# Optimization experiments

Hardware: AMD Instinct MI355X
Metric: run time of the kernel (lower is better)

## Reference

```python
import jax, jax.numpy as jnp
from jax import lax
import numpy as np

W_SSIM = 0.5
W_SMOOTH = 0.1
W_LR = 1.0
C1 = 0.01 ** 2
C2 = 0.03 ** 2


def avg3(x):
    # 3x3 stride-1 VALID average pool (matches F.avg_pool2d(x, 3, 1))
    return lax.reduce_window(x, 0.0, lax.add, (1, 1, 3, 3), (1, 1, 1, 1), 'VALID') / 9.0


def resize_ac(img, oh, ow):
    # bilinear resize with align_corners=True, separable gathers
    B, C, H, W = img.shape
    ys = jnp.linspace(0.0, H - 1.0, oh)
    xs = jnp.linspace(0.0, W - 1.0, ow)
    y0 = jnp.floor(ys).astype(jnp.int32); y1 = jnp.minimum(y0 + 1, H - 1); wy = ys - y0
    x0 = jnp.floor(xs).astype(jnp.int32); x1 = jnp.minimum(x0 + 1, W - 1); wx = xs - x0
    r = img[:, :, y0, :] * (1.0 - wy)[None, None, :, None] + img[:, :, y1, :] * wy[None, None, :, None]
    return r[:, :, :, x0] * (1.0 - wx) + r[:, :, :, x1] * wx


def warp_h(img, disp, sign):
    # horizontal bilinear warp: sample img at x + sign*disp (disp in units of image width),
    # align_corners=True pixel mapping, zeros padding outside the image.
    B, C, H, W = img.shape
    xb = jnp.linspace(0.0, 1.0, W)
    px = (xb[None, None, :] + sign * disp[:, 0, :, :]) * (W - 1)  # [B,H,W] pixel coords
    x0 = jnp.floor(px); f = px - x0
    x0i = x0.astype(jnp.int32); x1i = x0i + 1
    v0 = ((x0i >= 0) & (x0i < W)).astype(img.dtype)
    v1 = ((x1i >= 0) & (x1i < W)).astype(img.dtype)
    i0 = jnp.broadcast_to(jnp.clip(x0i, 0, W - 1)[:, None], (B, C, H, W))
    i1 = jnp.broadcast_to(jnp.clip(x1i, 0, W - 1)[:, None], (B, C, H, W))
    g0 = jnp.take_along_axis(img, i0, axis=3)
    g1 = jnp.take_along_axis(img, i1, axis=3)
    return g0 * (v0 * (1.0 - f))[:, None] + g1 * (v1 * f)[:, None]


def ssim(x, y):
    mu_x = avg3(x); mu_y = avg3(y)
    sig_x = avg3(x * x) - mu_x ** 2
    sig_y = avg3(y * y) - mu_y ** 2
    sig_xy = avg3(x * y) - mu_x * mu_y
    s = ((2 * mu_x * mu_y + C1) * (2 * sig_xy + C2)) / ((mu_x ** 2 + mu_y ** 2 + C1) * (sig_x + sig_y + C2))
    return jnp.clip((1.0 - s) / 2.0, 0.0, 1.0)


def smoothness(disp, img):
    dgx = disp[:, :, :, :-1] - disp[:, :, :, 1:]
    dgy = disp[:, :, :-1, :] - disp[:, :, 1:, :]
    igx = img[:, :, :, :-1] - img[:, :, :, 1:]
    igy = img[:, :, :-1, :] - img[:, :, 1:, :]
    wx = jnp.exp(-jnp.mean(jnp.abs(igx), axis=1, keepdims=True))
    wy = jnp.exp(-jnp.mean(jnp.abs(igy), axis=1, keepdims=True))
    return jnp.mean(jnp.abs(dgx * wx)) + jnp.mean(jnp.abs(dgy * wy))


def compute_loss(disps, left, right):
    B, _, H, W = left.shape
    img_loss = 0.0
    lr_loss = 0.0
    sm_loss = 0.0
    for i, d in enumerate(disps):
        r = 2 ** i
        h, w = H // r, W // r
        lpy = left if i == 0 else resize_ac(left, h, w)
        rpy = right if i == 0 else resize_ac(right, h, w)
        dl = d[:, 0:1]; dr = d[:, 1:2]
        left_est = warp_h(rpy, dl, -1.0)
        right_est = warp_h(lpy, dr, 1.0)
        rl_disp = warp_h(dr, dl, -1.0)
        lr_disp = warp_h(dl, dr, 1.0)
        l1_l = jnp.mean(jnp.abs(left_est - lpy))
        l1_r = jnp.mean(jnp.abs(right_est - rpy))
        ss_l = jnp.mean(ssim(left_est, lpy))
        ss_r = jnp.mean(ssim(right_est, rpy))
        img_loss = img_loss + W_SSIM * ss_l + (1 - W_SSIM) * l1_l + W_SSIM * ss_r + (1 - W_SSIM) * l1_r
        lr_loss = lr_loss + jnp.mean(jnp.abs(rl_disp - dl)) + jnp.mean(jnp.abs(lr_disp - dr))
        sm_loss = sm_loss + (smoothness(dl, lpy) + smoothness(dr, rpy)) / r
    return img_loss + W_SMOOTH * sm_loss + W_LR * lr_loss


def setup_inputs() -> dict:
    key = jax.random.key(0)
    ks = jax.random.split(key, 6)
    B, H, W = 16, 384, 768
    inp = {}
    for i in range(4):
        r = 2 ** i
        # disparities in units of image width; scaled to realistic ~[0, 0.1]
        inp[f'disp{i}'] = jax.random.uniform(ks[i], (B, 2, H // r, W // r), dtype=jnp.float32) * 0.1
    inp['left_image'] = jax.random.uniform(ks[4], (B, 3, H, W), dtype=jnp.float32)
    inp['right_image'] = jax.random.uniform(ks[5], (B, 3, H, W), dtype=jnp.float32)
    return inp


def reference(disp0, disp1, disp2, disp3, left_image, right_image):
    return compute_loss([disp0, disp1, disp2, disp3], left_image, right_image)
```

## Files before the change

kernel.cpp:

```cpp
#include <hip/hip_runtime.h>
#include <math.h>

#define C1F 1.0e-4f
#define C2F 9.0e-4f
#define TX 32
#define TY 8


struct ScaleArgs {
    const float* disp;
    const float* lp;
    const float* rp;
    int h, w, nx, ny, blk0;
};

__device__ __forceinline__ float2 f2(float v) { return make_float2(v, v); }
__device__ __forceinline__ float2 f2abs(float2 a) {
    return make_float2(fabsf(a.x), fabsf(a.y));
}

__device__ __forceinline__ void warp_coeffs(float px, int W, int& i0, int& i1,
                                            float& w0, float& w1) {
    float x0f = floorf(px);
    float f = px - x0f;
    int x0i = (int)x0f;
    int x1i = x0i + 1;
    float v0 = (x0i >= 0 && x0i < W) ? 1.f : 0.f;
    float v1 = (x1i >= 0 && x1i < W) ? 1.f : 0.f;
    i0 = min(max(x0i, 0), W - 1);
    i1 = min(max(x1i, 0), W - 1);
    w0 = v0 * (1.f - f);
    w1 = v1 * f;
}

template<int N>
__device__ __forceinline__ void block_acc(const float* vals, float* gacc) {
    __shared__ float sacc[N];
    if (threadIdx.x < N) sacc[threadIdx.x] = 0.f;
    __syncthreads();
#pragma unroll
    for (int k = 0; k < N; ++k) {
        float v = vals[k];
#pragma unroll
        for (int off = 32; off > 0; off >>= 1) v += __shfl_down(v, off, 64);
        if ((threadIdx.x & 63) == 0) atomicAdd(&sacc[k], v);
    }
    __syncthreads();
    if (threadIdx.x < N) atomicAdd(&gacc[threadIdx.x], sacc[threadIdx.x]);
}

__global__ void __launch_bounds__(256, 4)
k_resize_all(const float* __restrict__ left, const float* __restrict__ right,
             float* __restrict__ lo1, float* __restrict__ ro1,
             float* __restrict__ lo2, float* __restrict__ ro2,
             float* __restrict__ lo3, float* __restrict__ ro3,
             float* __restrict__ acc,
             int B, int H, int W,
             long long n1, long long n2, long long n3) {
    if (blockIdx.x == gridDim.x - 1 && threadIdx.x < 64) acc[threadIdx.x] = 0.f;
    long long idx = (long long)blockIdx.x * blockDim.x + threadIdx.x;
    int oh, ow;
    float* lo;
    float* ro;
    if (idx < n1) {
        oh = H / 2; ow = W / 2; lo = lo1; ro = ro1;
    } else if (idx < n1 + n2) {
        idx -= n1; oh = H / 4; ow = W / 4; lo = lo2; ro = ro2;
    } else if (idx < n1 + n2 + n3) {
        idx -= n1 + n2; oh = H / 8; ow = W / 8; lo = lo3; ro = ro3;
    } else {
        return;
    }
    long long half = (long long)B * 3 * oh * ow;
    const float* src = left;
    float* dst = lo;
    if (idx >= half) { src = right; dst = ro; idx -= half; }
    int x = (int)(idx % ow);
    long long t = idx / ow;
    int y = (int)(t % oh);
    t /= oh;
    int c = (int)(t % 3);
    int b = (int)(t / 3);
    float sy = (float)(H - 1) / (float)(oh - 1);
    float sx = (float)(W - 1) / (float)(ow - 1);
    float fy = y * sy;
    float fx = x * sx;
    int y0 = (int)floorf(fy); float wy = fy - (float)y0;
    int x0 = (int)floorf(fx); float wx = fx - (float)x0;
    int y1 = min(y0 + 1, H - 1); y0 = min(y0, H - 1);
    int x1 = min(x0 + 1, W - 1); x0 = min(x0, W - 1);
    const float* p = src + (((long long)b * 3 + c) * H) * W;
    float a00 = p[(long long)y0 * W + x0];
    float a10 = p[(long long)y1 * W + x0];
    float a01 = p[(long long)y0 * W + x1];
    float a11 = p[(long long)y1 * W + x1];
    float r0 = a00 * (1.f - wy) + a10 * wy;
    float r1 = a01 * (1.f - wy) + a11 * wy;
    dst[(((long long)b * 3 + c) * oh + y) * ow + x] = r0 * (1.f - wx) + r1 * wx;
}

__global__ void __launch_bounds__(256, 4)
k_fused_all(ScaleArgs s0, ScaleArgs s1, ScaleArgs s2, ScaleArgs s3,
            float* __restrict__ accbase) {
    __shared__ float4 simg[3][(TY + 2) * (TX + 2)];
    __shared__ float2 sdisp[(TY + 2) * (TX + 2)];

    ScaleArgs sa;
    int scale;
    {
        int blk = blockIdx.x;
        if (blk >= s3.blk0)      { sa = s3; scale = 3; }
        else if (blk >= s2.blk0) { sa = s2; scale = 2; }
        else if (blk >= s1.blk0) { sa = s1; scale = 1; }
        else                     { sa = s0; scale = 0; }
    }
    const int h = sa.h, w = sa.w;
    const float* __restrict__ disp = sa.disp;
    const float* __restrict__ lpy = sa.lp;
    const float* __restrict__ rpy = sa.rp;
    float* acc = accbase + scale * 8;

    int t = blockIdx.x - sa.blk0;
    const int tileX = t % sa.nx;
    int t2 = t / sa.nx;
    const int tileY = t2 % sa.ny;
    const int b = t2 / sa.ny;

    const int xo0 = tileX * TX;
    const int yo0 = tileY * TY;
    const int tid = threadIdx.x;
    const float Wm1 = (float)(w - 1);
    const float invWm1 = 1.f / Wm1;

    const float* dl_base = disp + ((long long)b * 2 + 0) * h * w;
    const float* dr_base = disp + ((long long)b * 2 + 1) * h * w;

    for (int i = tid; i < (TY + 2) * (TX + 2); i += 256) {
        int sx = i % (TX + 2);
        int sy = i / (TX + 2);
        int x = min(max(xo0 - 1 + sx, 0), w - 1);
        int y = min(max(yo0 - 1 + sy, 0), h - 1);
        const float* dl_row = dl_base + (long long)y * w;
        const float* dr_row = dr_base + (long long)y * w;
        float dl = dl_row[x], dr = dr_row[x];
        sdisp[i] = make_float2(dl, dr);
        float xb = (float)x * invWm1;
        int i0L, i1L; float w0L, w1L;
        warp_coeffs((xb - dl) * Wm1, w, i0L, i1L, w0L, w1L);
        int i0R, i1R; float w0R, w1R;
        warp_coeffs((xb + dr) * Wm1, w, i0R, i1R, w0R, w1R);
#pragma unroll
        for (int c = 0; c < 3; ++c) {
            const float* lrow = lpy + (((long long)b * 3 + c) * h + y) * w;
            const float* rrow = rpy + (((long long)b * 3 + c) * h + y) * w;
            float lv = lrow[x], rv = rrow[x];
            float le = rrow[i0L] * w0L + rrow[i1L] * w1L;
            float re = lrow[i0R] * w0R + lrow[i1R] * w1R;
            simg[c][i] = make_float4(le, re, lv, rv);
        }
    }
    __syncthreads();

    float sums[8] = {0.f, 0.f, 0.f, 0.f, 0.f, 0.f, 0.f, 0.f};
    const int tx = tid % TX, ty = tid / TX;
    const int x = xo0 + tx, y = yo0 + ty;
    if (x < w && y < h) {
        const int s = (ty + 1) * (TX + 2) + (tx + 1);
        float2 dd = sdisp[s];
        float dl = dd.x, dr = dd.y;
#pragma unroll
        for (int c = 0; c < 3; ++c) {
            float4 v = simg[c][s];
            float2 a = make_float2(v.x, v.y);
            float2 bb = make_float2(v.z, v.w);
            float2 d = f2abs(a - bb);
            sums[0] += d.x;
            sums[1] += d.y;
        }
        {
            float xb = (float)x * invWm1;
            int i0, i1; float w0, w1;
            warp_coeffs((xb - dl) * Wm1, w, i0, i1, w0, w1);
            const float* dr_row = dr_base + (long long)y * w;
            float rl = dr_row[i0] * w0 + dr_row[i1] * w1;
            sums[2] += fabsf(rl - dl);
            warp_coeffs((xb + dr) * Wm1, w, i0, i1, w0, w1);
            const float* dl_row = dl_base + (long long)y * w;
            float lr = dl_row[i0] * w0 + dl_row[i1] * w1;
            sums[3] += fabsf(lr - dr);
        }
        const float third = 1.f / 3.f;
        if (x < w - 1) {
            float2 d1 = sdisp[s + 1];
            float2 alr = f2(0.f);
#pragma unroll
            for (int c = 0; c < 3; ++c) {
                float4 v = simg[c][s];
                float4 v1 = simg[c][s + 1];
                alr = alr + f2abs(make_float2(v.z, v.w) - make_float2(v1.z, v1.w));
            }
            sums[4] += fabsf((dl - d1.x) * expf(-alr.x * third)) +
                       fabsf((dr - d1.y) * expf(-alr.y * third));
        }
        if (y < h - 1) {
            float2 d1 = sdisp[s + (TX + 2)];
            float2 alr = f2(0.f);
#pragma unroll
            for (int c = 0; c < 3; ++c) {
                float4 v = simg[c][s];
                float4 v1 = simg[c][s + (TX + 2)];
                alr = alr + f2abs(make_float2(v.z, v.w) - make_float2(v1.z, v1.w));
            }
            sums[5] += fabsf((dl - d1.x) * expf(-alr.x * third)) +
                       fabsf((dr - d1.y) * expf(-alr.y * third));
        }
        if (x >= 1 && x <= w - 2 && y >= 1 && y <= h - 2) {
            const float2 inv9 = f2(1.f / 9.f);
            const float2 c1 = f2(C1F), c2 = f2(C2F);
            const float2 two = f2(2.f), one = f2(1.f), half_ = f2(0.5f);
#pragma unroll 1
            for (int c = 0; c < 3; ++c) {
                float2 sX = f2(0.f), sY = f2(0.f);
                float2 sXX = f2(0.f), sYY = f2(0.f), sXY = f2(0.f);
#pragma unroll
                for (int dy = 0; dy < 3; ++dy) {
#pragma unroll
                    for (int dx = 0; dx < 3; ++dx) {
                        float4 v = simg[c][(ty + dy) * (TX + 2) + (tx + dx)];
                        float2 a = make_float2(v.x, v.y);
                        float2 bb = make_float2(v.z, v.w);
                        sX = sX + a;
                        sY = sY + bb;
                        sXX = sXX + a * a;
                        sYY = sYY + bb * bb;
                        sXY = sXY + a * bb;
                    }
                }
                float2 mx = sX * inv9, my = sY * inv9;
                float2 vx = sXX * inv9 - mx * mx;
                float2 vy = sYY * inv9 - my * my;
                float2 vxy = sXY * inv9 - mx * my;
                float2 num = (two * mx * my + c1) * (two * vxy + c2);
                float2 den = (mx * mx + my * my + c1) * (vx + vy + c2);
                float2 ss = make_float2(num.x / den.x, num.y / den.y);
                float2 v = (one - ss) * half_;
                sums[6] += fminf(fmaxf(v.x, 0.f), 1.f);
                sums[7] += fminf(fmaxf(v.y, 0.f), 1.f);
            }
        }
    }
    block_acc<8>(sums, acc);
}

__global__ void k_final(const float* __restrict__ acc, float* __restrict__ out,
                        int B, int H, int W) {
    if (threadIdx.x != 0 || blockIdx.x != 0) return;
    float img = 0.f, lr = 0.f, sm = 0.f;
    for (int i = 0; i < 4; ++i) {
        int r = 1 << i;
        int h = H / r, w = W / r;
        const float* a = acc + i * 8;
        float Nl1 = (float)B * 3.f * (float)h * (float)w;
        float Nss = (float)B * 3.f * (float)(h - 2) * (float)(w - 2);
        float Nlr = (float)B * (float)h * (float)w;
        float Nsx = (float)B * (float)h * (float)(w - 1);
        float Nsy = (float)B * (float)(h - 1) * (float)w;
        img += 0.5f * (a[6] / Nss) + 0.5f * (a[0] / Nl1)
             + 0.5f * (a[7] / Nss) + 0.5f * (a[1] / Nl1);
        lr += a[2] / Nlr + a[3] / Nlr;
        sm += (a[4] / Nsx + a[5] / Nsy) / (float)r;
    }
    out[0] = img + 0.1f * sm + 1.0f * lr;
}

extern "C" void kernel_launch(void* const* d_in, const int* in_sizes, int n_in,
                              void* d_out, int out_size, void* d_ws, size_t ws_size,
                              hipStream_t stream) {
    const int B = 16, H = 384, W = 768;
    const float* disp[4] = {(const float*)d_in[0], (const float*)d_in[1],
                            (const float*)d_in[2], (const float*)d_in[3]};
    const float* left = (const float*)d_in[4];
    const float* right = (const float*)d_in[5];
    float* out = (float*)d_out;

    float* acc = (float*)d_ws;
    float* pyr = acc + 256;
    long long sz1 = (long long)B * 3 * (H / 2) * (W / 2);
    long long sz2 = (long long)B * 3 * (H / 4) * (W / 4);
    long long sz3 = (long long)B * 3 * (H / 8) * (W / 8);
    float* lp1 = pyr;
    float* rp1 = lp1 + sz1;
    float* lp2 = rp1 + sz1;
    float* rp2 = lp2 + sz2;
    float* lp3 = rp2 + sz2;
    float* rp3 = lp3 + sz3;

    const int TB = 256;

    {
        long long n1 = 2 * sz1, n2 = 2 * sz2, n3 = 2 * sz3;
        long long nt = n1 + n2 + n3;
        hipLaunchKernelGGL(k_resize_all, dim3((unsigned)((nt + TB - 1) / TB)), dim3(TB), 0, stream,
                           left, right, lp1, rp1, lp2, rp2, lp3, rp3, acc,
                           B, H, W, n1, n2, n3);
    }

    {
        const float* lp[4] = {left, lp1, lp2, lp3};
        const float* rp[4] = {right, rp1, rp2, rp3};
        ScaleArgs sa[4];
        int blk0 = 0;
        for (int i = 0; i < 4; ++i) {
            int r = 1 << i;
            int h = H / r, w = W / r;
            sa[i].disp = disp[i];
            sa[i].lp = lp[i];
            sa[i].rp = rp[i];
            sa[i].h = h;
            sa[i].w = w;
            sa[i].nx = w / TX;
            sa[i].ny = h / TY;
            sa[i].blk0 = blk0;
            blk0 += sa[i].nx * sa[i].ny * B;
        }
        hipLaunchKernelGGL(k_fused_all, dim3((unsigned)blk0), dim3(TB), 0, stream,
                           sa[0], sa[1], sa[2], sa[3], acc);
    }
    hipLaunchKernelGGL(k_final, dim3(1), dim3(64), 0, stream, acc, out, B, H, W);
}
```

Measured before the change: 506.0 us.

## Fuse pyramid resize into loss kernel, sampling full-res images on the fly

Result: slower. 542.3 us (+7.2%).

```diff
diff --git a/kernel.cpp b/kernel.cpp
--- a/kernel.cpp
+++ b/kernel.cpp
@@ -9,8 +9,6 @@
 
 struct ScaleArgs {
     const float* disp;
-    const float* lp;
-    const float* rp;
     int h, w, nx, ny, blk0;
 };
 
@@ -33,6 +31,41 @@
     w1 = v1 * f;
 }
 
+__device__ __forceinline__ float3 bil3(const float* __restrict__ img,
+                                       long long bOff, long long cStride,
+                                       int FW, int y0, int y1, float wy,
+                                       int xs, float sx) {
+    float fx = (float)xs * sx;
+    int x0 = (int)floorf(fx);
+    float wx = fx - (float)x0;
+    int x1 = min(x0 + 1, FW - 1);
+    x0 = min(x0, FW - 1);
+    const float* p0 = img + bOff + (long long)y0 * FW;
+    const float* p1 = img + bOff + (long long)y1 * FW;
+    float3 r;
+    {
+        float a00 = p0[x0], a10 = p1[x0], a01 = p0[x1], a11 = p1[x1];
+        float r0 = a00 * (1.f - wy) + a10 * wy;
+        float r1 = a01 * (1.f - wy) + a11 * wy;
+        r.x = r0 * (1.f - wx) + r1 * wx;
+    }
+    p0 += cStride; p1 += cStride;
+    {
+        float a00 = p0[x0], a10 = p1[x0], a01 = p0[x1], a11 = p1[x1];
+        float r0 = a00 * (1.f - wy) + a10 * wy;
+        float r1 = a01 * (1.f - wy) + a11 * wy;
+        r.y = r0 * (1.f - wx) + r1 * wx;
+    }
+    p0 += cStride; p1 += cStride;
+    {
+        float a00 = p0[x0], a10 = p1[x0], a01 = p0[x1], a11 = p1[x1];
+        float r0 = a00 * (1.f - wy) + a10 * wy;
+        float r1 = a01 * (1.f - wy) + a11 * wy;
+        r.z = r0 * (1.f - wx) + r1 * wx;
+    }
+    return r;
+}
+
 template<int N>
 __device__ __forceinline__ void block_acc(const float* vals, float* gacc) {
     __shared__ float sacc[N];
@@ -49,59 +82,14 @@
     if (threadIdx.x < N) atomicAdd(&gacc[threadIdx.x], sacc[threadIdx.x]);
 }
 
-__global__ void __launch_bounds__(256, 4)
-k_resize_all(const float* __restrict__ left, const float* __restrict__ right,
-             float* __restrict__ lo1, float* __restrict__ ro1,
-             float* __restrict__ lo2, float* __restrict__ ro2,
-             float* __restrict__ lo3, float* __restrict__ ro3,
-             float* __restrict__ acc,
-             int B, int H, int W,
-             long long n1, long long n2, long long n3) {
-    if (blockIdx.x == gridDim.x - 1 && threadIdx.x < 64) acc[threadIdx.x] = 0.f;
-    long long idx = (long long)blockIdx.x * blockDim.x + threadIdx.x;
-    int oh, ow;
-    float* lo;
-    float* ro;
-    if (idx < n1) {
-        oh = H / 2; ow = W / 2; lo = lo1; ro = ro1;
-    } else if (idx < n1 + n2) {
-        idx -= n1; oh = H / 4; ow = W / 4; lo = lo2; ro = ro2;
-    } else if (idx < n1 + n2 + n3) {
-        idx -= n1 + n2; oh = H / 8; ow = W / 8; lo = lo3; ro = ro3;
-    } else {
-        return;
-    }
-    long long half = (long long)B * 3 * oh * ow;
-    const float* src = left;
-    float* dst = lo;
-    if (idx >= half) { src = right; dst = ro; idx -= half; }
-    int x = (int)(idx % ow);
-    long long t = idx / ow;
-    int y = (int)(t % oh);
-    t /= oh;
-    int c = (int)(t % 3);
-    int b = (int)(t / 3);
-    float sy = (float)(H - 1) / (float)(oh - 1);
-    float sx = (float)(W - 1) / (float)(ow - 1);
-    float fy = y * sy;
-    float fx = x * sx;
-    int y0 = (int)floorf(fy); float wy = fy - (float)y0;
-    int x0 = (int)floorf(fx); float wx = fx - (float)x0;
-    int y1 = min(y0 + 1, H - 1); y0 = min(y0, H - 1);
-    int x1 = min(x0 + 1, W - 1); x0 = min(x0, W - 1);
-    const float* p = src + (((long long)b * 3 + c) * H) * W;
-    float a00 = p[(long long)y0 * W + x0];
-    float a10 = p[(long long)y1 * W + x0];
-    float a01 = p[(long long)y0 * W + x1];
-    float a11 = p[(long long)y1 * W + x1];
-    float r0 = a00 * (1.f - wy) + a10 * wy;
-    float r1 = a01 * (1.f - wy) + a11 * wy;
-    dst[(((long long)b * 3 + c) * oh + y) * ow + x] = r0 * (1.f - wx) + r1 * wx;
+__global__ void k_zero(float* acc) {
+    if (threadIdx.x < 64) acc[threadIdx.x] = 0.f;
 }
 
 __global__ void __launch_bounds__(256, 4)
 k_fused_all(ScaleArgs s0, ScaleArgs s1, ScaleArgs s2, ScaleArgs s3,
-            float* __restrict__ accbase) {
+            const float* __restrict__ fleft, const float* __restrict__ fright,
+            int FH, int FW, float* __restrict__ accbase) {
     __shared__ float4 simg[3][(TY + 2) * (TX + 2)];
     __shared__ float2 sdisp[(TY + 2) * (TX + 2)];
 
@@ -116,8 +104,6 @@
     }
     const int h = sa.h, w = sa.w;
     const float* __restrict__ disp = sa.disp;
-    const float* __restrict__ lpy = sa.lp;
-    const float* __restrict__ rpy = sa.rp;
     float* acc = accbase + scale * 8;
 
     int t = blockIdx.x - sa.blk0;
@@ -134,12 +120,14 @@
 
     const float* dl_base = disp + ((long long)b * 2 + 0) * h * w;
     const float* dr_base = disp + ((long long)b * 2 + 1) * h * w;
+    const long long cStride = (long long)FH * FW;
+    const long long bOff = (long long)b * 3 * cStride;
 
     for (int i = tid; i < (TY + 2) * (TX + 2); i += 256) {
-        int sx = i % (TX + 2);
-        int sy = i / (TX + 2);
-        int x = min(max(xo0 - 1 + sx, 0), w - 1);
-        int y = min(max(yo0 - 1 + sy, 0), h - 1);
+        int sx_ = i % (TX + 2);
+        int sy_ = i / (TX + 2);
+        int x = min(max(xo0 - 1 + sx_, 0), w - 1);
+        int y = min(max(yo0 - 1 + sy_, 0), h - 1);
         const float* dl_row = dl_base + (long long)y * w;
         const float* dr_row = dr_base + (long long)y * w;
         float dl = dl_row[x], dr = dr_row[x];
@@ -149,14 +137,36 @@
         warp_coeffs((xb - dl) * Wm1, w, i0L, i1L, w0L, w1L);
         int i0R, i1R; float w0R, w1R;
         warp_coeffs((xb + dr) * Wm1, w, i0R, i1R, w0R, w1R);
-#pragma unroll
-        for (int c = 0; c < 3; ++c) {
-            const float* lrow = lpy + (((long long)b * 3 + c) * h + y) * w;
-            const float* rrow = rpy + (((long long)b * 3 + c) * h + y) * w;
-            float lv = lrow[x], rv = rrow[x];
-            float le = rrow[i0L] * w0L + rrow[i1L] * w1L;
-            float re = lrow[i0R] * w0R + lrow[i1R] * w1R;
-            simg[c][i] = make_float4(le, re, lv, rv);
+        if (scale == 0) {
+#pragma unroll
+            for (int c = 0; c < 3; ++c) {
+                const float* lrow = fleft + bOff + c * cStride + (long long)y * FW;
+                const float* rrow = fright + bOff + c * cStride + (long long)y * FW;
+                float lv = lrow[x], rv = rrow[x];
+                float le = rrow[i0L] * w0L + rrow[i1L] * w1L;
+                float re = lrow[i0R] * w0R + lrow[i1R] * w1R;
+                simg[c][i] = make_float4(le, re, lv, rv);
+            }
+        } else {
+            float syc = (float)(FH - 1) / (float)(h - 1);
+            float sxc = (float)(FW - 1) / (float)(w - 1);
+            float fy = (float)y * syc;
+            int y0 = (int)floorf(fy);
+            float wy = fy - (float)y0;
+            int y1 = min(y0 + 1, FH - 1);
+            y0 = min(y0, FH - 1);
+            float3 lv3 = bil3(fleft, bOff, cStride, FW, y0, y1, wy, x, sxc);
+            float3 rv3 = bil3(fright, bOff, cStride, FW, y0, y1, wy, x, sxc);
+            float3 rg0 = bil3(fright, bOff, cStride, FW, y0, y1, wy, i0L, sxc);
+            float3 rg1 = bil3(fright, bOff, cStride, FW, y0, y1, wy, i1L, sxc);
+            float3 lg0 = bil3(fleft, bOff, cStride, FW, y0, y1, wy, i0R, sxc);
+            float3 lg1 = bil3(fleft, bOff, cStride, FW, y0, y1, wy, i1R, sxc);
+            simg[0][i] = make_float4(rg0.x * w0L + rg1.x * w1L,
+                                     lg0.x * w0R + lg1.x * w1R, lv3.x, rv3.x);
+            simg[1][i] = make_float4(rg0.y * w0L + rg1.y * w1L,
+                                     lg0.y * w0R + lg1.y * w1R, lv3.y, rv3.y);
+            simg[2][i] = make_float4(rg0.z * w0L + rg1.z * w1L,
+                                     lg0.z * w0R + lg1.z * w1R, lv3.z, rv3.z);
         }
     }
     __syncthreads();
@@ -282,40 +292,18 @@
     const float* left = (const float*)d_in[4];
     const float* right = (const float*)d_in[5];
     float* out = (float*)d_out;
-
     float* acc = (float*)d_ws;
-    float* pyr = acc + 256;
-    long long sz1 = (long long)B * 3 * (H / 2) * (W / 2);
-    long long sz2 = (long long)B * 3 * (H / 4) * (W / 4);
-    long long sz3 = (long long)B * 3 * (H / 8) * (W / 8);
-    float* lp1 = pyr;
-    float* rp1 = lp1 + sz1;
-    float* lp2 = rp1 + sz1;
-    float* rp2 = lp2 + sz2;
-    float* lp3 = rp2 + sz2;
-    float* rp3 = lp3 + sz3;
 
     const int TB = 256;
-
-    {
-        long long n1 = 2 * sz1, n2 = 2 * sz2, n3 = 2 * sz3;
-        long long nt = n1 + n2 + n3;
-        hipLaunchKernelGGL(k_resize_all, dim3((unsigned)((nt + TB - 1) / TB)), dim3(TB), 0, stream,
-                           left, right, lp1, rp1, lp2, rp2, lp3, rp3, acc,
-                           B, H, W, n1, n2, n3);
-    }
-
-    {
-        const float* lp[4] = {left, lp1, lp2, lp3};
-        const float* rp[4] = {right, rp1, rp2, rp3};
+    hipLaunchKernelGGL(k_zero, dim3(1), dim3(64), 0, stream, acc);
+
+    {
         ScaleArgs sa[4];
         int blk0 = 0;
         for (int i = 0; i < 4; ++i) {
             int r = 1 << i;
             int h = H / r, w = W / r;
             sa[i].disp = disp[i];
-            sa[i].lp = lp[i];
-            sa[i].rp = rp[i];
             sa[i].h = h;
             sa[i].w = w;
             sa[i].nx = w / TX;
@@ -324,7 +312,7 @@
             blk0 += sa[i].nx * sa[i].ny * B;
         }
         hipLaunchKernelGGL(k_fused_all, dim3((unsigned)blk0), dim3(TB), 0, stream,
-                           sa[0], sa[1], sa[2], sa[3], acc);
+                           sa[0], sa[1], sa[2], sa[3], left, right, H, W, acc);
     }
     hipLaunchKernelGGL(k_final, dim3(1), dim3(64), 0, stream, acc, out, B, H, W);
 }
```

## Overlap full-resolution loss tiles with pyramid resize in one launch

Applied to the files above, without the earlier changes.

After: 514.0 us. No clear change (+1.6%).

```diff
diff --git a/kernel.cpp b/kernel.cpp
--- a/kernel.cpp
+++ b/kernel.cpp
@@ -11,7 +11,7 @@
     const float* disp;
     const float* lp;
     const float* rp;
-    int h, w, nx, ny, blk0;
+    int h, w, nx, ny, blk0, accoff;
 };
 
 __device__ __forceinline__ float2 f2(float v) { return make_float2(v, v); }
@@ -49,16 +49,164 @@
     if (threadIdx.x < N) atomicAdd(&gacc[threadIdx.x], sacc[threadIdx.x]);
 }
 
+__global__ void k_zero(float* acc) {
+    if (threadIdx.x < 64) acc[threadIdx.x] = 0.f;
+}
+
+__device__ __forceinline__ void fused_tile(const ScaleArgs& sa, int t,
+                                           float* __restrict__ accbase) {
+    __shared__ float4 simg[3][(TY + 2) * (TX + 2)];
+    __shared__ float2 sdisp[(TY + 2) * (TX + 2)];
+
+    const int h = sa.h, w = sa.w;
+    const float* __restrict__ disp = sa.disp;
+    const float* __restrict__ lpy = sa.lp;
+    const float* __restrict__ rpy = sa.rp;
+    float* acc = accbase + sa.accoff;
+
+    const int tileX = t % sa.nx;
+    int t2 = t / sa.nx;
+    const int tileY = t2 % sa.ny;
+    const int b = t2 / sa.ny;
+
+    const int xo0 = tileX * TX;
+    const int yo0 = tileY * TY;
+    const int tid = threadIdx.x;
+    const float Wm1 = (float)(w - 1);
+    const float invWm1 = 1.f / Wm1;
+
+    const float* dl_base = disp + ((long long)b * 2 + 0) * h * w;
+    const float* dr_base = disp + ((long long)b * 2 + 1) * h * w;
+
+    for (int i = tid; i < (TY + 2) * (TX + 2); i += 256) {
+        int sx = i % (TX + 2);
+        int sy = i / (TX + 2);
+        int x = min(max(xo0 - 1 + sx, 0), w - 1);
+        int y = min(max(yo0 - 1 + sy, 0), h - 1);
+        const float* dl_row = dl_base + (long long)y * w;
+        const float* dr_row = dr_base + (long long)y * w;
+        float dl = dl_row[x], dr = dr_row[x];
+        sdisp[i] = make_float2(dl, dr);
+        float xb = (float)x * invWm1;
+        int i0L, i1L; float w0L, w1L;
+        warp_coeffs((xb - dl) * Wm1, w, i0L, i1L, w0L, w1L);
+        int i0R, i1R; float w0R, w1R;
+        warp_coeffs((xb + dr) * Wm1, w, i0R, i1R, w0R, w1R);
+#pragma unroll
+        for (int c = 0; c < 3; ++c) {
+            const float* lrow = lpy + (((long long)b * 3 + c) * h + y) * w;
+            const float* rrow = rpy + (((long long)b * 3 + c) * h + y) * w;
+            float lv = lrow[x], rv = rrow[x];
+            float le = rrow[i0L] * w0L + rrow[i1L] * w1L;
+            float re = lrow[i0R] * w0R + lrow[i1R] * w1R;
+            simg[c][i] = make_float4(le, re, lv, rv);
+        }
+    }
+    __syncthreads();
+
+    float sums[8] = {0.f, 0.f, 0.f, 0.f, 0.f, 0.f, 0.f, 0.f};
+    const int tx = tid % TX, ty = tid / TX;
+    const int x = xo0 + tx, y = yo0 + ty;
+    if (x < w && y < h) {
+        const int s = (ty + 1) * (TX + 2) + (tx + 1);
+        float2 dd = sdisp[s];
+        float dl = dd.x, dr = dd.y;
+#pragma unroll
+        for (int c = 0; c < 3; ++c) {
+            float4 v = simg[c][s];
+            float2 d = f2abs(make_float2(v.x, v.y) - make_float2(v.z, v.w));
+            sums[0] += d.x;
+            sums[1] += d.y;
+        }
+        {
+            float xb = (float)x * invWm1;
+            int i0, i1; float w0, w1;
+            warp_coeffs((xb - dl) * Wm1, w, i0, i1, w0, w1);
+            const float* dr_row = dr_base + (long long)y * w;
+            float rl = dr_row[i0] * w0 + dr_row[i1] * w1;
+            sums[2] += fabsf(rl - dl);
+            warp_coeffs((xb + dr) * Wm1, w, i0, i1, w0, w1);
+            const float* dl_row = dl_base + (long long)y * w;
+            float lr = dl_row[i0] * w0 + dl_row[i1] * w1;
+            sums[3] += fabsf(lr - dr);
+        }
+        const float third = 1.f / 3.f;
+        if (x < w - 1) {
+            float2 d1 = sdisp[s + 1];
+            float2 alr = f2(0.f);
+#pragma unroll
+            for (int c = 0; c < 3; ++c) {
+                float4 v = simg[c][s];
+                float4 v1 = simg[c][s + 1];
+                alr = alr + f2abs(make_float2(v.z, v.w) - make_float2(v1.z, v1.w));
+            }
+            sums[4] += fabsf((dl - d1.x) * expf(-alr.x * third)) +
+                       fabsf((dr - d1.y) * expf(-alr.y * third));
+        }
+        if (y < h - 1) {
+            float2 d1 = sdisp[s + (TX + 2)];
+            float2 alr = f2(0.f);
+#pragma unroll
+            for (int c = 0; c < 3; ++c) {
+                float4 v = simg[c][s];
+                float4 v1 = simg[c][s + (TX + 2)];
+                alr = alr + f2abs(make_float2(v.z, v.w) - make_float2(v1.z, v1.w));
+            }
+            sums[5] += fabsf((dl - d1.x) * expf(-alr.x * third)) +
+                       fabsf((dr - d1.y) * expf(-alr.y * third));
+        }
+        if (x >= 1 && x <= w - 2 && y >= 1 && y <= h - 2) {
+            const float2 inv9 = f2(1.f / 9.f);
+            const float2 c1 = f2(C1F), c2 = f2(C2F);
+            const float2 two = f2(2.f), one = f2(1.f), half_ = f2(0.5f);
+#pragma unroll 1
+            for (int c = 0; c < 3; ++c) {
+                float2 sX = f2(0.f), sY = f2(0.f);
+                float2 sXX = f2(0.f), sYY = f2(0.f), sXY = f2(0.f);
+#pragma unroll
+                for (int dy = 0; dy < 3; ++dy) {
+#pragma unroll
+                    for (int dx = 0; dx < 3; ++dx) {
+                        float4 v = simg[c][(ty + dy) * (TX + 2) + (tx + dx)];
+                        float2 a = make_float2(v.x, v.y);
+                        float2 bb = make_float2(v.z, v.w);
+                        sX = sX + a;
+                        sY = sY + bb;
+                        sXX = sXX + a * a;
+                        sYY = sYY + bb * bb;
+                        sXY = sXY + a * bb;
+                    }
+                }
+                float2 mx = sX * inv9, my = sY * inv9;
+                float2 vx = sXX * inv9 - mx * mx;
+                float2 vy = sYY * inv9 - my * my;
+                float2 vxy = sXY * inv9 - mx * my;
+                float2 num = (two * mx * my + c1) * (two * vxy + c2);
+                float2 den = (mx * mx + my * my + c1) * (vx + vy + c2);
+                float2 ss = make_float2(num.x / den.x, num.y / den.y);
+                float2 v = (one - ss) * half_;
+                sums[6] += fminf(fmaxf(v.x, 0.f), 1.f);
+                sums[7] += fminf(fmaxf(v.y, 0.f), 1.f);
+            }
+        }
+    }
+    block_acc<8>(sums, accbase + sa.accoff - sa.accoff + sa.accoff);
+    (void)acc;
+}
+
 __global__ void __launch_bounds__(256, 4)
-k_resize_all(const float* __restrict__ left, const float* __restrict__ right,
-             float* __restrict__ lo1, float* __restrict__ ro1,
-             float* __restrict__ lo2, float* __restrict__ ro2,
-             float* __restrict__ lo3, float* __restrict__ ro3,
-             float* __restrict__ acc,
-             int B, int H, int W,
-             long long n1, long long n2, long long n3) {
-    if (blockIdx.x == gridDim.x - 1 && threadIdx.x < 64) acc[threadIdx.x] = 0.f;
-    long long idx = (long long)blockIdx.x * blockDim.x + threadIdx.x;
+k_fused0_resize(ScaleArgs s0, float* __restrict__ accbase,
+                const float* __restrict__ left, const float* __restrict__ right,
+                float* __restrict__ lo1, float* __restrict__ ro1,
+                float* __restrict__ lo2, float* __restrict__ ro2,
+                float* __restrict__ lo3, float* __restrict__ ro3,
+                int B, int H, int W,
+                int nFusedBlocks, long long n1, long long n2, long long n3) {
+    if ((int)blockIdx.x < nFusedBlocks) {
+        fused_tile(s0, blockIdx.x, accbase);
+        return;
+    }
+    long long idx = (long long)(blockIdx.x - nFusedBlocks) * blockDim.x + threadIdx.x;
     int oh, ow;
     float* lo;
     float* ro;
@@ -100,156 +248,16 @@
 }
 
 __global__ void __launch_bounds__(256, 4)
-k_fused_all(ScaleArgs s0, ScaleArgs s1, ScaleArgs s2, ScaleArgs s3,
-            float* __restrict__ accbase) {
-    __shared__ float4 simg[3][(TY + 2) * (TX + 2)];
-    __shared__ float2 sdisp[(TY + 2) * (TX + 2)];
-
+k_fused_small(ScaleArgs s1, ScaleArgs s2, ScaleArgs s3,
+              float* __restrict__ accbase) {
     ScaleArgs sa;
-    int scale;
     {
         int blk = blockIdx.x;
-        if (blk >= s3.blk0)      { sa = s3; scale = 3; }
-        else if (blk >= s2.blk0) { sa = s2; scale = 2; }
-        else if (blk >= s1.blk0) { sa = s1; scale = 1; }
-        else                     { sa = s0; scale = 0; }
-    }
-    const int h = sa.h, w = sa.w;
-    const float* __restrict__ disp = sa.disp;
-    const float* __restrict__ lpy = sa.lp;
-    const float* __restrict__ rpy = sa.rp;
-    float* acc = accbase + scale * 8;
-
-    int t = blockIdx.x - sa.blk0;
-    const int tileX = t % sa.nx;
-    int t2 = t / sa.nx;
-    const int tileY = t2 % sa.ny;
-    const int b = t2 / sa.ny;
-
-    const int xo0 = tileX * TX;
-    const int yo0 = tileY * TY;
-    const int tid = threadIdx.x;
-    const float Wm1 = (float)(w - 1);
-    const float invWm1 = 1.f / Wm1;
-
-    const float* dl_base = disp + ((long long)b * 2 + 0) * h * w;
-    const float* dr_base = disp + ((long long)b * 2 + 1) * h * w;
-
-    for (int i = tid; i < (TY + 2) * (TX + 2); i += 256) {
-        int sx = i % (TX + 2);
-        int sy = i / (TX + 2);
-        int x = min(max(xo0 - 1 + sx, 0), w - 1);
-        int y = min(max(yo0 - 1 + sy, 0), h - 1);
-        const float* dl_row = dl_base + (long long)y * w;
-        const float* dr_row = dr_base + (long long)y * w;
-        float dl = dl_row[x], dr = dr_row[x];
-        sdisp[i] = make_float2(dl, dr);
-        float xb = (float)x * invWm1;
-        int i0L, i1L; float w0L, w1L;
-        warp_coeffs((xb - dl) * Wm1, w, i0L, i1L, w0L, w1L);
-        int i0R, i1R; float w0R, w1R;
-        warp_coeffs((xb + dr) * Wm1, w, i0R, i1R, w0R, w1R);
-#pragma unroll
-        for (int c = 0; c < 3; ++c) {
-            const float* lrow = lpy + (((long long)b * 3 + c) * h + y) * w;
-            const float* rrow = rpy + (((long long)b * 3 + c) * h + y) * w;
-            float lv = lrow[x], rv = rrow[x];
-            float le = rrow[i0L] * w0L + rrow[i1L] * w1L;
-            float re = lrow[i0R] * w0R + lrow[i1R] * w1R;
-            simg[c][i] = make_float4(le, re, lv, rv);
-        }
-    }
-    __syncthreads();
-
-    float sums[8] = {0.f, 0.f, 0.f, 0.f, 0.f, 0.f, 0.f, 0.f};
-    const int tx = tid % TX, ty = tid / TX;
-    const int x = xo0 + tx, y = yo0 + ty;
-    if (x < w && y < h) {
-        const int s = (ty + 1) * (TX + 2) + (tx + 1);
-        float2 dd = sdisp[s];
-        float dl = dd.x, dr = dd.y;
-#pragma unroll
-        for (int c = 0; c < 3; ++c) {
-            float4 v = simg[c][s];
-            float2 a = make_float2(v.x, v.y);
-            float2 bb = make_float2(v.z, v.w);
-            float2 d = f2abs(a - bb);
-            sums[0] += d.x;
-            sums[1] += d.y;
-        }
-        {
-            float xb = (float)x * invWm1;
-            int i0, i1; float w0, w1;
-            warp_coeffs((xb - dl) * Wm1, w, i0, i1, w0, w1);
-            const float* dr_row = dr_base + (long long)y * w;
-            float rl = dr_row[i0] * w0 + dr_row[i1] * w1;
-            sums[2] += fabsf(rl - dl);
-            warp_coeffs((xb + dr) * Wm1, w, i0, i1, w0, w1);
-            const float* dl_row = dl_base + (long long)y * w;
-            float lr = dl_row[i0] * w0 + dl_row[i1] * w1;
-            sums[3] += fabsf(lr - dr);
-        }
-        const float third = 1.f / 3.f;
-        if (x < w - 1) {
-            float2 d1 = sdisp[s + 1];
-            float2 alr = f2(0.f);
-#pragma unroll
-            for (int c = 0; c < 3; ++c) {
-                float4 v = simg[c][s];
-                float4 v1 = simg[c][s + 1];
-                alr = alr + f2abs(make_float2(v.z, v.w) - make_float2(v1.z, v1.w));
-            }
-            sums[4] += fabsf((dl - d1.x) * expf(-alr.x * third)) +
-                       fabsf((dr - d1.y) * expf(-alr.y * third));
-        }
-        if (y < h - 1) {
-            float2 d1 = sdisp[s + (TX + 2)];
-            float2 alr = f2(0.f);
-#pragma unroll
-            for (int c = 0; c < 3; ++c) {
-                float4 v = simg[c][s];
-                float4 v1 = simg[c][s + (TX + 2)];
-                alr = alr + f2abs(make_float2(v.z, v.w) - make_float2(v1.z, v1.w));
-            }
-            sums[5] += fabsf((dl - d1.x) * expf(-alr.x * third)) +
-                       fabsf((dr - d1.y) * expf(-alr.y * third));
-        }
-        if (x >= 1 && x <= w - 2 && y >= 1 && y <= h - 2) {
-            const float2 inv9 = f2(1.f / 9.f);
-            const float2 c1 = f2(C1F), c2 = f2(C2F);
-            const float2 two = f2(2.f), one = f2(1.f), half_ = f2(0.5f);
-#pragma unroll 1
-            for (int c = 0; c < 3; ++c) {
-                float2 sX = f2(0.f), sY = f2(0.f);
-                float2 sXX = f2(0.f), sYY = f2(0.f), sXY = f2(0.f);
-#pragma unroll
-                for (int dy = 0; dy < 3; ++dy) {
-#pragma unroll
-                    for (int dx = 0; dx < 3; ++dx) {
-                        float4 v = simg[c][(ty + dy) * (TX + 2) + (tx + dx)];
-                        float2 a = make_float2(v.x, v.y);
-                        float2 bb = make_float2(v.z, v.w);
-                        sX = sX + a;
-                        sY = sY + bb;
-                        sXX = sXX + a * a;
-                        sYY = sYY + bb * bb;
-                        sXY = sXY + a * bb;
-                    }
-                }
-                float2 mx = sX * inv9, my = sY * inv9;
-                float2 vx = sXX * inv9 - mx * mx;
-                float2 vy = sYY * inv9 - my * my;
-                float2 vxy = sXY * inv9 - mx * my;
-                float2 num = (two * mx * my + c1) * (two * vxy + c2);
-                float2 den = (mx * mx + my * my + c1) * (vx + vy + c2);
-                float2 ss = make_float2(num.x / den.x, num.y / den.y);
-                float2 v = (one - ss) * half_;
-                sums[6] += fminf(fmaxf(v.x, 0.f), 1.f);
-                sums[7] += fminf(fmaxf(v.y, 0.f), 1.f);
-            }
-        }
-    }
-    block_acc<8>(sums, acc);
+        if (blk >= s3.blk0)      sa = s3;
+        else if (blk >= s2.blk0) sa = s2;
+        else                     sa = s1;
+    }
+    fused_tile(sa, blockIdx.x - sa.blk0, accbase);
 }
 
 __global__ void k_final(const float* __restrict__ acc, float* __restrict__ out,
@@ -296,35 +304,44 @@
     float* rp3 = lp3 + sz3;
 
     const int TB = 256;
+    const float* lp[4] = {left, lp1, lp2, lp3};
+    const float* rp[4] = {right, rp1, rp2, rp3};
+    ScaleArgs sa[4];
+    for (int i = 0; i < 4; ++i) {
+        int r = 1 << i;
+        int h = H / r, w = W / r;
+        sa[i].disp = disp[i];
+        sa[i].lp = lp[i];
+        sa[i].rp = rp[i];
+        sa[i].h = h;
+        sa[i].w = w;
+        sa[i].nx = w / TX;
+        sa[i].ny = h / TY;
+        sa[i].accoff = i * 8;
+        sa[i].blk0 = 0;
+    }
+
+    hipLaunchKernelGGL(k_zero, dim3(1), dim3(64), 0, stream, acc);
 
     {
+        int nFused = sa[0].nx * sa[0].ny * B;
         long long n1 = 2 * sz1, n2 = 2 * sz2, n3 = 2 * sz3;
-        long long nt = n1 + n2 + n3;
-        hipLaunchKernelGGL(k_resize_all, dim3((unsigned)((nt + TB - 1) / TB)), dim3(TB), 0, stream,
-                           left, right, lp1, rp1, lp2, rp2, lp3, rp3, acc,
-                           B, H, W, n1, n2, n3);
+        long long nrElem = n1 + n2 + n3;
+        int nResize = (int)((nrElem + TB - 1) / TB);
+        hipLaunchKernelGGL(k_fused0_resize, dim3((unsigned)(nFused + nResize)), dim3(TB), 0, stream,
+                           sa[0], acc, left, right, lp1, rp1, lp2, rp2, lp3, rp3,
+                           B, H, W, nFused, n1, n2, n3);
     }
 
     {
-        const float* lp[4] = {left, lp1, lp2, lp3};
-        const float* rp[4] = {right, rp1, rp2, rp3};
-        ScaleArgs sa[4];
-        int blk0 = 0;
-        for (int i = 0; i < 4; ++i) {
-            int r = 1 << i;
-            int h = H / r, w = W / r;
-            sa[i].disp = disp[i];
-            sa[i].lp = lp[i];
-            sa[i].rp = rp[i];
-            sa[i].h = h;
-            sa[i].w = w;
-            sa[i].nx = w / TX;
-            sa[i].ny = h / TY;
-            sa[i].blk0 = blk0;
-            blk0 += sa[i].nx * sa[i].ny * B;
-        }
-        hipLaunchKernelGGL(k_fused_all, dim3((unsigned)blk0), dim3(TB), 0, stream,
-                           sa[0], sa[1], sa[2], sa[3], acc);
+        int b1 = sa[1].nx * sa[1].ny * B;
+        int b2 = sa[2].nx * sa[2].ny * B;
+        int b3 = sa[3].nx * sa[3].ny * B;
+        sa[1].blk0 = 0;
+        sa[2].blk0 = b1;
+        sa[3].blk0 = b1 + b2;
+        hipLaunchKernelGGL(k_fused_small, dim3((unsigned)(b1 + b2 + b3)), dim3(TB), 0, stream,
+                           sa[1], sa[2], sa[3], acc);
     }
     hipLaunchKernelGGL(k_final, dim3(1), dim3(64), 0, stream, acc, out, B, H, W);
 }
```
